# Optimization experiments

Hardware: AMD Instinct MI355X
Metric: run time of the kernel (lower is better)

Reference implementation:

```python
import jax, jax.numpy as jnp
import numpy as np

N, T, D = 2, 4096, 1024
HD = 64          # head_dim
NH = D // HD     # 16 heads
W = 128          # sliding window size
BASE = 10000.0
EPS = 1.1920929e-07  # torch F.rms_norm default eps = float32 eps


def setup_inputs() -> dict:
    key = jax.random.key(0)
    k1, k2, k3, k4 = jax.random.split(key, 4)
    return {
        "input_NTD": jax.random.normal(k1, (N, T, D), jnp.float32),
        "qkv_weight": jax.random.normal(k2, (3, D, D), jnp.float32) / (D ** 0.5) / 2.0,
        "o_weight": jax.random.normal(k3, (D, D), jnp.float32) / (D ** 0.5) * 0.5,
        "o_scale": jax.random.normal(k4, (D,), jnp.float32) * 0.02,
    }


def _rms(x):
    x = x.astype(jnp.float32)
    return x * jax.lax.rsqrt(jnp.mean(x * x, axis=-1, keepdims=True) + EPS)


def reference(input_NTD, qkv_weight, o_weight, o_scale):
    # RMSNorm + fused QKV
    x = _rms(input_NTD)
    qkv = x @ qkv_weight.reshape(3 * D, D).T            # [N,T,3D]
    qkv = qkv.reshape(N, T, 3 * NH, HD)
    q, k, v = jnp.split(qkv, 3, axis=2)                 # each [N,T,NH,HD]
    q, k = _rms(q), _rms(k)
    # Rotary: freqs over head_dim//4 then zero-padded to head_dim//2
    nf = HD // 4
    freqs = (1.0 / BASE) ** jnp.linspace(0.0, 1.0, nf)
    freqs_d = jnp.concatenate([freqs, jnp.zeros_like(freqs)])       # [HD//2]
    theta = jnp.arange(T, dtype=jnp.float32)[:, None] * freqs_d     # [T,HD//2]
    cos = jnp.cos(theta)[None, :, None, :]
    sin = jnp.sin(theta)[None, :, None, :]
    def rot(z):
        z1, z2 = jnp.split(z, 2, axis=-1)
        return jnp.concatenate([z1 * cos + z2 * sin, -z1 * sin + z2 * cos], axis=-1)
    q, k = rot(q), rot(k)
    # [N,NH,T,HD] -> chunked sliding-window attention (chunk = W tokens)
    qh = q.transpose(0, 2, 1, 3)
    kh = k.transpose(0, 2, 1, 3)
    vh = v.transpose(0, 2, 1, 3).astype(jnp.float32)
    C = T // W
    qc = qh.reshape(N, NH, C, W, HD)
    kc = kh.reshape(N, NH, C, W, HD)
    vc = vh.reshape(N, NH, C, W, HD)
    kprev = jnp.concatenate([jnp.zeros_like(kc[:, :, :1]), kc[:, :, :-1]], axis=2)
    vprev = jnp.concatenate([jnp.zeros_like(vc[:, :, :1]), vc[:, :, :-1]], axis=2)
    kp = jnp.concatenate([kprev, kc], axis=3)           # [N,NH,C,2W,HD]
    vp = jnp.concatenate([vprev, vc], axis=3)
    scores = jnp.einsum('nhcqd,nhckd->nhcqk', qc, kp) / jnp.sqrt(jnp.float32(HD))
    j = jnp.arange(W)[:, None]
    m = jnp.arange(2 * W)[None, :]
    base = (m > j) & (m <= W + j)                       # 0 <= qpos-kpos < W
    chunk_ok = (jnp.arange(C)[:, None, None] > 0) | (m[None] >= W)
    mask = base[None] & chunk_ok                        # [C,W,2W]
    scores = jnp.where(mask[None, None], scores, -jnp.inf)
    probs = jax.nn.softmax(scores, axis=-1)
    out = jnp.einsum('nhcqk,nhckd->nhcqd', probs, vp)   # [N,NH,C,W,HD]
    out = out.reshape(N, NH, T, HD).transpose(0, 2, 1, 3).reshape(N, T, D)
    out = out.astype(input_NTD.dtype)
    # o_proj: FusedLinear with per-output scale, no bias
    o = out @ (o_weight * o_scale[:, None]).T
    return input_NTD + o
```

## Files before the change

kernel.cpp:

```cpp
#include <hip/hip_runtime.h>
#include <hip/hip_bf16.h>
#include <stdint.h>
#include <stddef.h>

#define T_S 4096
#define D_M 1024
#define NH_ 16
#define EPSF 1.1920929e-07f

typedef float f32x4 __attribute__((ext_vector_type(4)));
typedef __bf16 bf16x8 __attribute__((ext_vector_type(8)));
typedef short short8 __attribute__((ext_vector_type(8)));
typedef unsigned short ushort4v __attribute__((ext_vector_type(4)));

static __device__ __forceinline__ unsigned short f2bf(float f) {
  unsigned int u = __builtin_bit_cast(unsigned int, f);
  unsigned int r = (u + 0x7fffu + ((u >> 16) & 1u)) >> 16;
  return (unsigned short)r;
}

#define GLDS16(gp, lp) __builtin_amdgcn_global_load_lds( \
    (__attribute__((address_space(1))) void*)(gp),       \
    (__attribute__((address_space(3))) void*)(lp), 16, 0, 0)

static __device__ __forceinline__ f32x4 mfma16(bf16x8 a, bf16x8 b, f32x4 c) {
  return __builtin_amdgcn_mfma_f32_16x16x32_bf16(a, b, c, 0, 0, 0);
}

__global__ __launch_bounds__(256) void k_rope_tab(float* __restrict__ cosT,
                                                  float* __restrict__ sinT) {
  int i = blockIdx.x * 256 + threadIdx.x;
  int t = i >> 5, f = i & 31;
  float fr = (f < 16) ? powf(1e-4f, (float)f * (1.0f / 15.0f)) : 0.0f;
  float th = (float)t * fr;
  cosT[i] = cosf(th);
  sinT[i] = sinf(th);
}

__global__ __launch_bounds__(256) void k_f32_to_bf16(const float* __restrict__ src,
                                                     unsigned short* __restrict__ dst) {
  int i = blockIdx.x * 256 + threadIdx.x;
  float4 v = ((const float4*)src)[i];
  ushort4v o;
  o.x = f2bf(v.x); o.y = f2bf(v.y); o.z = f2bf(v.z); o.w = f2bf(v.w);
  ((ushort4v*)dst)[i] = o;
}

__global__ __launch_bounds__(256) void k_rmsnorm_cast(const float* __restrict__ x,
                                                      unsigned short* __restrict__ xn) {
  const int row = blockIdx.x;
  const int tid = threadIdx.x;
  float4 v = ((const float4*)(x + (size_t)row * D_M))[tid];
  float ss = v.x * v.x + v.y * v.y + v.z * v.z + v.w * v.w;
#pragma unroll
  for (int d = 1; d < 64; d <<= 1) ss += __shfl_xor(ss, d, 64);
  __shared__ float red[4];
  if ((tid & 63) == 0) red[tid >> 6] = ss;
  __syncthreads();
  float sc = rsqrtf((red[0] + red[1] + red[2] + red[3]) * (1.0f / D_M) + EPSF);
  ushort4v o;
  o.x = f2bf(v.x * sc); o.y = f2bf(v.y * sc); o.z = f2bf(v.z * sc); o.w = f2bf(v.w * sc);
  ((ushort4v*)(xn + (size_t)row * D_M))[tid] = o;
}

template <int EPI>
__global__ __launch_bounds__(512, 2) void k_gemm2p(
    const unsigned short* __restrict__ A, const unsigned short* __restrict__ B,
    unsigned short* __restrict__ q_out, unsigned short* __restrict__ k_out,
    unsigned short* __restrict__ v_out, float* __restrict__ Cf,
    const float* __restrict__ resid, const float* __restrict__ scale,
    const float* __restrict__ cosT, const float* __restrict__ sinT,
    int cpx) {
  extern __shared__ __align__(16) char lds[];
  const int tid = threadIdx.x;
  const int lane = tid & 63, w = tid >> 6;
  const int lrow = lane & 15, g4 = lane >> 4;
  const int wm = w >> 2, wn = w & 3;
  const int id = (blockIdx.x & 7) * cpx + (blockIdx.x >> 3);
  const int m0 = (id & 63) * 128, n0 = (id >> 6) * 256;

  auto stA = [&](int t, int kh, int dbx) {
    const int sg = ((tid & 3) ^ ((tid >> 3) & 3)) << 3;
    const unsigned short* s =
        A + (size_t)(m0 + (tid >> 2)) * 1024 + t * 64 + kh * 32 + sg;
    GLDS16(s, lds + dbx * 49152 + kh * 8192 + tid * 16);
  };
  auto stB = [&](int t, int kh, int dbx) {
#pragma unroll
    for (int it = 0; it < 2; ++it) {
      int ci = it * 512 + tid;
      const int sg = ((ci & 3) ^ ((ci >> 3) & 3)) << 3;
      const unsigned short* s =
          B + (size_t)(n0 + (ci >> 2)) * 1024 + t * 64 + kh * 32 + sg;
      GLDS16(s, lds + dbx * 49152 + 16384 + kh * 16384 + ci * 16);
    }
  };

  int a_off[2][4], b_off[2][4];
#pragma unroll
  for (int kh = 0; kh < 2; ++kh) {
#pragma unroll
    for (int i = 0; i < 4; ++i) {
      int ar = wm * 64 + i * 16 + lrow;
      a_off[kh][i] = kh * 8192 + ar * 64 + ((g4 ^ ((ar >> 1) & 3)) << 4);
      int br = wn * 64 + i * 16 + lrow;
      b_off[kh][i] = 16384 + kh * 16384 + br * 64 + ((g4 ^ ((br >> 1) & 3)) << 4);
    }
  }

  f32x4 acc[4][4] = {};

  stA(0, 0, 0); stB(0, 0, 0);
  stA(0, 1, 0); stB(0, 1, 0);
  stA(1, 0, 1); stB(1, 0, 1);
  asm volatile("s_waitcnt vmcnt(3)" ::: "memory");
  __builtin_amdgcn_s_barrier();
  asm volatile("" ::: "memory");

  for (int T = 0; T < 16; ++T) {
    const int db = T & 1;
    const char* cp = lds + db * 49152;
    {
      bf16x8 aF[4], bF[4];
#pragma unroll
      for (int i = 0; i < 4; ++i) aF[i] = *(const bf16x8*)(cp + a_off[0][i]);
#pragma unroll
      for (int i = 0; i < 4; ++i) bF[i] = *(const bf16x8*)(cp + b_off[0][i]);
      if (T < 15) { stA(T + 1, 1, db ^ 1); stB(T + 1, 1, db ^ 1); }
      __builtin_amdgcn_s_setprio(1);
#pragma unroll
      for (int mi = 0; mi < 4; ++mi)
#pragma unroll
        for (int ni = 0; ni < 4; ++ni)
          acc[mi][ni] = mfma16(aF[mi], bF[ni], acc[mi][ni]);
      __builtin_amdgcn_s_setprio(0);
      asm volatile("" ::: "memory");
      __builtin_amdgcn_s_barrier();
      asm volatile("" ::: "memory");
    }
    {
      bf16x8 aF[4], bF[4];
#pragma unroll
      for (int i = 0; i < 4; ++i) aF[i] = *(const bf16x8*)(cp + a_off[1][i]);
#pragma unroll
      for (int i = 0; i < 4; ++i) bF[i] = *(const bf16x8*)(cp + b_off[1][i]);
      if (T < 14) { stA(T + 2, 0, db); stB(T + 2, 0, db); }
      __builtin_amdgcn_s_setprio(1);
#pragma unroll
      for (int mi = 0; mi < 4; ++mi)
#pragma unroll
        for (int ni = 0; ni < 4; ++ni)
          acc[mi][ni] = mfma16(aF[mi], bF[ni], acc[mi][ni]);
      __builtin_amdgcn_s_setprio(0);
      if (T < 14)
        asm volatile("s_waitcnt vmcnt(3)" ::: "memory");
      else
        asm volatile("s_waitcnt vmcnt(0)" ::: "memory");
      __builtin_amdgcn_s_barrier();
      asm volatile("" ::: "memory");
    }
  }

  const int rbase = m0 + wm * 64 + g4 * 4;
  const int colbase = n0 + wn * 64;

  if (EPI == 1) {
#pragma unroll
    for (int mi = 0; mi < 4; ++mi)
#pragma unroll
      for (int nf = 0; nf < 4; ++nf) {
        int col = colbase + nf * 16 + lrow;
        float sc = scale[col];
#pragma unroll
        for (int j = 0; j < 4; ++j) {
          int row = rbase + mi * 16 + j;
          size_t idx = (size_t)row * 1024 + col;
          Cf[idx] = resid[idx] + sc * acc[mi][nf][j];
        }
      }
  } else {
    const int which = colbase >> 10;
    const int hh = (colbase >> 6) & 15;
    if (which == 2) {
#pragma unroll
      for (int mi = 0; mi < 4; ++mi)
#pragma unroll
        for (int j = 0; j < 4; ++j) {
          int row = rbase + mi * 16 + j;
          int t = row & (T_S - 1), nn = row >> 12;
          size_t ob = ((size_t)(nn * NH_ + hh) * T_S + t) * 64;
#pragma unroll
          for (int nf = 0; nf < 4; ++nf)
            v_out[ob + nf * 16 + lrow] = f2bf(acc[mi][nf][j]);
        }
    } else {
      unsigned short* dst = which ? k_out : q_out;
#pragma unroll
      for (int mi = 0; mi < 4; ++mi)
#pragma unroll
        for (int j = 0; j < 4; ++j) {
          int row = rbase + mi * 16 + j;
          int t = row & (T_S - 1), nn = row >> 12;
          float ss = 0.0f;
#pragma unroll
          for (int nf = 0; nf < 4; ++nf) ss += acc[mi][nf][j] * acc[mi][nf][j];
          ss += __shfl_xor(ss, 1, 64);
          ss += __shfl_xor(ss, 2, 64);
          ss += __shfl_xor(ss, 4, 64);
          ss += __shfl_xor(ss, 8, 64);
          float sc = rsqrtf(ss * (1.0f / 64.0f) + EPSF);
          size_t ob = ((size_t)(nn * NH_ + hh) * T_S + t) * 64;
#pragma unroll
          for (int nf = 0; nf < 2; ++nf) {
            int dd = nf * 16 + lrow;
            float cs = cosT[t * 32 + dd], sn = sinT[t * 32 + dd];
            float z1 = acc[mi][nf][j] * sc, z2 = acc[mi][nf + 2][j] * sc;
            dst[ob + dd] = f2bf(z1 * cs + z2 * sn);
            dst[ob + dd + 32] = f2bf(z2 * cs - z1 * sn);
          }
        }
    }
  }
}

__global__ __launch_bounds__(256) void k_attn(const unsigned short* __restrict__ qh,
                                              const unsigned short* __restrict__ kh,
                                              const unsigned short* __restrict__ vh,
                                              unsigned short* __restrict__ ao) {
  extern __shared__ __align__(16) char lds[];
  unsigned short* Vt = (unsigned short*)lds;
  unsigned short* Pb = (unsigned short*)(lds + 64 * 264 * 2);
  const int b = blockIdx.x;
  const int c = b & 31, nh = b >> 5;
  const int tid = threadIdx.x, lane = tid & 63, w = tid >> 6;
  const int lrow = lane & 15, g = lane >> 4, lk8 = g * 8;
  const size_t hb = (size_t)nh * T_S * 64;
  const unsigned short* qg = qh + hb + (size_t)c * 128 * 64;
  const unsigned short* kg = kh + hb + ((ptrdiff_t)c * 128 - 128) * 64;
  const unsigned short* vg = vh + hb + ((ptrdiff_t)c * 128 - 128) * 64;

  {
    const int m_idx = (tid & 7) | ((tid >> 6) << 3);
    const int m0v = m_idx * 8;
    const int d0 = ((tid >> 3) & 7) * 8;
    short8 vv[8];
#pragma unroll
    for (int i = 0; i < 8; ++i) {
      short8 z = {0, 0, 0, 0, 0, 0, 0, 0};
      if (!(c == 0 && m0v < 128)) z = *(const short8*)(vg + (size_t)(m0v + i) * 64 + d0);
      vv[i] = z;
    }
#pragma unroll
    for (int jj = 0; jj < 8; ++jj) {
      short8 wv;
#pragma unroll
      for (int i = 0; i < 8; ++i) wv[i] = vv[i][jj];
      *(short8*)(Vt + (size_t)(d0 + jj) * 264 + m0v) = wv;
    }
  }

  bf16x8 qf[2][2];
#pragma unroll
  for (int mi = 0; mi < 2; ++mi)
#pragma unroll
    for (int ks = 0; ks < 2; ++ks)
      qf[mi][ks] =
          *(const bf16x8*)(qg + (size_t)(w * 32 + mi * 16 + lrow) * 64 + ks * 32 + lk8);

  const int nlo = 2 * w;
  f32x4 s[2][10] = {};
#pragma unroll
  for (int u = 0; u < 10; ++u) {
    const int ni = nlo + u;
    if (c == 0 && ni < 8) continue;
    bf16x8 kf0 = *(const bf16x8*)(kg + (size_t)(ni * 16 + lrow) * 64 + lk8);
    bf16x8 kf1 = *(const bf16x8*)(kg + (size_t)(ni * 16 + lrow) * 64 + 32 + lk8);
#pragma unroll
    for (int mi = 0; mi < 2; ++mi) {
      s[mi][u] = mfma16(qf[mi][0], kf0, s[mi][u]);
      s[mi][u] = mfma16(qf[mi][1], kf1, s[mi][u]);
    }
  }

  float invs[2][4];
#pragma unroll
  for (int mi = 0; mi < 2; ++mi) {
#pragma unroll
    for (int j = 0; j < 4; ++j) {
      int jq = w * 32 + mi * 16 + g * 4 + j;
      float mx = -1e30f;
#pragma unroll
      for (int u = 0; u < 10; ++u) {
        int m = (nlo + u) * 16 + lrow;
        bool ok = (m > jq) && (m <= 128 + jq) && (c > 0 || m >= 128);
        float val = ok ? s[mi][u][j] * 0.125f : -1e30f;
        s[mi][u][j] = val;
        mx = fmaxf(mx, val);
      }
#pragma unroll
      for (int d2 = 1; d2 < 16; d2 <<= 1) mx = fmaxf(mx, __shfl_xor(mx, d2, 64));
      float sum = 0.0f;
#pragma unroll
      for (int u = 0; u < 10; ++u) {
        float p = __expf(s[mi][u][j] - mx);
        s[mi][u][j] = p;
        sum += p;
      }
#pragma unroll
      for (int d2 = 1; d2 < 16; d2 <<= 1) sum += __shfl_xor(sum, d2, 64);
      invs[mi][j] = 1.0f / sum;
    }
  }

  __syncthreads();

  f32x4 oacc[2][4] = {};
  unsigned short* Pw = Pb + w * (32 * 72);
  const int qlo = w >> 1;
#pragma unroll
  for (int qq = 0; qq < 3; ++qq) {
#pragma unroll
    for (int mi = 0; mi < 2; ++mi)
#pragma unroll
      for (int ni4 = 0; ni4 < 4; ++ni4)
#pragma unroll
        for (int j = 0; j < 4; ++j) {
          int r = mi * 16 + g * 4 + j;
          float val;
          if ((w & 1) == 0) {
            int u = qq * 4 + ni4;
            val = (u < 10) ? s[mi][u < 10 ? u : 0][j] : 0.0f;
          } else {
            int u = qq * 4 + ni4 - 2;
            val = (u >= 0 && u < 10) ? s[mi][(u >= 0 && u < 10) ? u : 0][j] : 0.0f;
          }
          Pw[r * 72 + ni4 * 16 + lrow] = f2bf(val);
        }
    const int qi = qlo + qq;
#pragma unroll
    for (int ks = 0; ks < 2; ++ks) {
      bf16x8 pf[2], vf[4];
#pragma unroll
      for (int mi = 0; mi < 2; ++mi)
        pf[mi] = *(const bf16x8*)&Pw[(mi * 16 + lrow) * 72 + ks * 32 + lk8];
#pragma unroll
      for (int nj = 0; nj < 4; ++nj)
        vf[nj] = *(const bf16x8*)&Vt[(nj * 16 + lrow) * 264 + qi * 64 + ks * 32 + lk8];
#pragma unroll
      for (int mi = 0; mi < 2; ++mi)
#pragma unroll
        for (int nj = 0; nj < 4; ++nj)
          oacc[mi][nj] = mfma16(pf[mi], vf[nj], oacc[mi][nj]);
    }
  }

  const int t0 = c * 128 + w * 32;
  const int n_ = nh >> 4, h_ = nh & 15;
#pragma unroll
  for (int mi = 0; mi < 2; ++mi)
#pragma unroll
    for (int nj = 0; nj < 4; ++nj)
#pragma unroll
      for (int j = 0; j < 4; ++j) {
        int t = t0 + mi * 16 + g * 4 + j;
        int dcol = nj * 16 + lrow;
        ao[((size_t)n_ * T_S + t) * D_M + h_ * 64 + dcol] =
            f2bf(oacc[mi][nj][j] * invs[mi][j]);
      }
}

extern "C" void kernel_launch(void* const* d_in, const int* in_sizes, int n_in,
                              void* d_out, int out_size, void* d_ws, size_t ws_size,
                              hipStream_t stream) {
  const float* x = (const float*)d_in[0];
  const float* qkvw = (const float*)d_in[1];
  const float* ow = (const float*)d_in[2];
  const float* osc = (const float*)d_in[3];
  float* out = (float*)d_out;

  char* ws = (char*)d_ws;
  unsigned short* xn = (unsigned short*)(ws + 0);
  unsigned short* qkvwb = (unsigned short*)(ws + 16777216);
  unsigned short* owb = (unsigned short*)(ws + 23068672);
  unsigned short* qhb = (unsigned short*)(ws + 25165824);
  unsigned short* khb = (unsigned short*)(ws + 41943040);
  unsigned short* vhb = (unsigned short*)(ws + 58720256);
  unsigned short* aob = (unsigned short*)(ws + 75497472);
  float* cosT = (float*)(ws + 92274688);
  float* sinT = (float*)(ws + 92798976);

  k_rope_tab<<<512, 256, 0, stream>>>(cosT, sinT);
  k_f32_to_bf16<<<3072, 256, 0, stream>>>(qkvw, qkvwb);
  k_f32_to_bf16<<<1024, 256, 0, stream>>>(ow, owb);
  k_rmsnorm_cast<<<8192, 256, 0, stream>>>(x, xn);
  k_gemm2p<0><<<768, 512, 98304, stream>>>(xn, qkvwb, qhb, khb, vhb, nullptr,
                                           nullptr, nullptr, cosT, sinT, 96);
  k_attn<<<1024, 256, 52224, stream>>>(qhb, khb, vhb, aob);
  k_gemm2p<1><<<256, 512, 98304, stream>>>(aob, owb, nullptr, nullptr, nullptr, out,
                                           x, osc, nullptr, nullptr, 32);
}
```

Measured before the change: 151.1 us.

## Triple-buffer GEMM LDS stages with one barrier per full K tile

The shared GEMM kernel moves from a double-buffered, half-K-step pipeline with two barriers per K tile to a three-buffer ring. Each iteration issues the whole prefetch for tile T+2 up front, then runs both K halves of MFMAs on the current buffer, with one waitcnt and one barrier per tile. This is meant to hide global-load latency deeper and halve barrier overhead in both the QKV and output projections. The cost is 144KB of LDS per block instead of 96KB, and more fragment registers held live at once.

```diff
diff --git a/kernel.cpp b/kernel.cpp
--- a/kernel.cpp
+++ b/kernel.cpp
@@ -64,7 +64,7 @@
 }
 
 template <int EPI>
-__global__ __launch_bounds__(512, 2) void k_gemm2p(
+__global__ __launch_bounds__(512, 2) void k_gemm3b(
     const unsigned short* __restrict__ A, const unsigned short* __restrict__ B,
     unsigned short* __restrict__ q_out, unsigned short* __restrict__ k_out,
     unsigned short* __restrict__ v_out, float* __restrict__ Cf,
@@ -79,20 +79,20 @@
   const int id = (blockIdx.x & 7) * cpx + (blockIdx.x >> 3);
   const int m0 = (id & 63) * 128, n0 = (id >> 6) * 256;
 
-  auto stA = [&](int t, int kh, int dbx) {
-    const int sg = ((tid & 3) ^ ((tid >> 3) & 3)) << 3;
-    const unsigned short* s =
-        A + (size_t)(m0 + (tid >> 2)) * 1024 + t * 64 + kh * 32 + sg;
-    GLDS16(s, lds + dbx * 49152 + kh * 8192 + tid * 16);
-  };
-  auto stB = [&](int t, int kh, int dbx) {
+  auto stage = [&](int t, int bb) {
+    const int sgA = ((tid & 3) ^ ((tid >> 3) & 3)) << 3;
+    const unsigned short* sa = A + (size_t)(m0 + (tid >> 2)) * 1024 + t * 64 + sgA;
+#pragma unroll
+    for (int kh = 0; kh < 2; ++kh)
+      GLDS16(sa + kh * 32, lds + bb + kh * 8192 + tid * 16);
 #pragma unroll
     for (int it = 0; it < 2; ++it) {
       int ci = it * 512 + tid;
       const int sg = ((ci & 3) ^ ((ci >> 3) & 3)) << 3;
-      const unsigned short* s =
-          B + (size_t)(n0 + (ci >> 2)) * 1024 + t * 64 + kh * 32 + sg;
-      GLDS16(s, lds + dbx * 49152 + 16384 + kh * 16384 + ci * 16);
+      const unsigned short* sb = B + (size_t)(n0 + (ci >> 2)) * 1024 + t * 64 + sg;
+#pragma unroll
+      for (int kh = 0; kh < 2; ++kh)
+        GLDS16(sb + kh * 32, lds + bb + 16384 + kh * 16384 + ci * 16);
     }
   };
 
@@ -110,55 +110,41 @@
 
   f32x4 acc[4][4] = {};
 
-  stA(0, 0, 0); stB(0, 0, 0);
-  stA(0, 1, 0); stB(0, 1, 0);
-  stA(1, 0, 1); stB(1, 0, 1);
-  asm volatile("s_waitcnt vmcnt(3)" ::: "memory");
+  stage(0, 0);
+  stage(1, 49152);
+  asm volatile("s_waitcnt vmcnt(6)" ::: "memory");
   __builtin_amdgcn_s_barrier();
   asm volatile("" ::: "memory");
 
+  int cb = 0, sb = 98304;
   for (int T = 0; T < 16; ++T) {
-    const int db = T & 1;
-    const char* cp = lds + db * 49152;
-    {
-      bf16x8 aF[4], bF[4];
-#pragma unroll
-      for (int i = 0; i < 4; ++i) aF[i] = *(const bf16x8*)(cp + a_off[0][i]);
-#pragma unroll
-      for (int i = 0; i < 4; ++i) bF[i] = *(const bf16x8*)(cp + b_off[0][i]);
-      if (T < 15) { stA(T + 1, 1, db ^ 1); stB(T + 1, 1, db ^ 1); }
-      __builtin_amdgcn_s_setprio(1);
+    if (T < 14) stage(T + 2, sb);
+    const char* cp = lds + cb;
+    bf16x8 aF[2][4], bF[2][4];
+#pragma unroll
+    for (int kh = 0; kh < 2; ++kh) {
+#pragma unroll
+      for (int i = 0; i < 4; ++i) aF[kh][i] = *(const bf16x8*)(cp + a_off[kh][i]);
+#pragma unroll
+      for (int i = 0; i < 4; ++i) bF[kh][i] = *(const bf16x8*)(cp + b_off[kh][i]);
+    }
+    __builtin_amdgcn_s_setprio(1);
+#pragma unroll
+    for (int kh = 0; kh < 2; ++kh)
 #pragma unroll
       for (int mi = 0; mi < 4; ++mi)
 #pragma unroll
         for (int ni = 0; ni < 4; ++ni)
-          acc[mi][ni] = mfma16(aF[mi], bF[ni], acc[mi][ni]);
-      __builtin_amdgcn_s_setprio(0);
-      asm volatile("" ::: "memory");
-      __builtin_amdgcn_s_barrier();
-      asm volatile("" ::: "memory");
-    }
-    {
-      bf16x8 aF[4], bF[4];
-#pragma unroll
-      for (int i = 0; i < 4; ++i) aF[i] = *(const bf16x8*)(cp + a_off[1][i]);
-#pragma unroll
-      for (int i = 0; i < 4; ++i) bF[i] = *(const bf16x8*)(cp + b_off[1][i]);
-      if (T < 14) { stA(T + 2, 0, db); stB(T + 2, 0, db); }
-      __builtin_amdgcn_s_setprio(1);
-#pragma unroll
-      for (int mi = 0; mi < 4; ++mi)
-#pragma unroll
-        for (int ni = 0; ni < 4; ++ni)
-          acc[mi][ni] = mfma16(aF[mi], bF[ni], acc[mi][ni]);
-      __builtin_amdgcn_s_setprio(0);
-      if (T < 14)
-        asm volatile("s_waitcnt vmcnt(3)" ::: "memory");
-      else
-        asm volatile("s_waitcnt vmcnt(0)" ::: "memory");
-      __builtin_amdgcn_s_barrier();
-      asm volatile("" ::: "memory");
-    }
+          acc[mi][ni] = mfma16(aF[kh][mi], bF[kh][ni], acc[mi][ni]);
+    __builtin_amdgcn_s_setprio(0);
+    if (T < 14)
+      asm volatile("s_waitcnt vmcnt(6)" ::: "memory");
+    else
+      asm volatile("s_waitcnt vmcnt(0)" ::: "memory");
+    __builtin_amdgcn_s_barrier();
+    asm volatile("" ::: "memory");
+    cb += 49152; if (cb == 147456) cb = 0;
+    sb += 49152; if (sb == 147456) sb = 0;
   }
 
   const int rbase = m0 + wm * 64 + g4 * 4;
@@ -393,9 +379,9 @@
   k_f32_to_bf16<<<3072, 256, 0, stream>>>(qkvw, qkvwb);
   k_f32_to_bf16<<<1024, 256, 0, stream>>>(ow, owb);
   k_rmsnorm_cast<<<8192, 256, 0, stream>>>(x, xn);
-  k_gemm2p<0><<<768, 512, 98304, stream>>>(xn, qkvwb, qhb, khb, vhb, nullptr,
-                                           nullptr, nullptr, cosT, sinT, 96);
+  k_gemm3b<0><<<768, 512, 147456, stream>>>(xn, qkvwb, qhb, khb, vhb, nullptr,
+                                            nullptr, nullptr, cosT, sinT, 96);
   k_attn<<<1024, 256, 52224, stream>>>(qhb, khb, vhb, aob);
-  k_gemm2p<1><<<256, 512, 98304, stream>>>(aob, owb, nullptr, nullptr, nullptr, out,
-                                           x, osc, nullptr, nullptr, 32);
-}
+  k_gemm3b<1><<<256, 512, 147456, stream>>>(aob, owb, nullptr, nullptr, nullptr, out,
+                                            x, osc, nullptr, nullptr, 32);
+}
```

Result: no change. 150.7 us (-0.3%).
